# Kernel tuning notes

Measured on AMD Instinct MI355X. Metric: run time of the kernel, lower is better.

## Reference

```python
import jax, jax.numpy as jnp
import numpy as np

B, X, Y, Z, CIN = 4, 64, 64, 64, 32
COUT = 32
MX, MY, MZ = 16, 16, 16


def setup_inputs() -> dict:
    key = jax.random.key(0)
    k1, k2, k3 = jax.random.split(key, 3)
    x = jax.random.normal(k1, (B, X, Y, Z, CIN), dtype=jnp.float32)
    # Glorot-uniform-like scale for (in, out, mx, my, mz) weights
    fan = CIN + COUT
    lim = np.sqrt(6.0 / fan).astype(np.float32)
    w_real = jax.random.uniform(k2, (CIN, COUT, MX, MY, MZ), minval=-lim, maxval=lim, dtype=jnp.float32)
    w_imag = jax.random.uniform(k3, (CIN, COUT, MX, MY, MZ), minval=-lim, maxval=lim, dtype=jnp.float32)
    return {"x": x, "w_real": w_real, "w_imag": w_imag}


def reference(x, w_real, w_imag):
    # tf.signal.fft3d transforms the innermost 3 axes of the 5D input:
    # x is [B, X, Y, Z, C] so the FFT runs over (Y, Z, C) -- faithful to source.
    x_ft = jnp.fft.fftn(x.astype(jnp.complex64), axes=(-3, -2, -1))
    x_ft = jnp.transpose(x_ft, (0, 4, 1, 2, 3))            # [B, C, X, Y, Z]
    mx, my, mz = w_real.shape[2], w_real.shape[3], w_real.shape[4]
    x_crop = x_ft[:, :, :mx, :my, :mz]                     # [B, Cin, mx, my, mz]
    w = jax.lax.complex(w_real, w_imag)                    # [Cin, Cout, mx, my, mz]
    out_ft = jnp.einsum('bixyz,ioxyz->boxyz', x_crop, w)   # [B, Cout, mx, my, mz]
    sx, sy, sz = x.shape[1], x.shape[2], x.shape[3]
    out_ft = jnp.pad(out_ft, ((0, 0), (0, 0), (0, sx - mx), (0, sy - my), (0, sz - mz)))
    out_ft = jnp.transpose(out_ft, (0, 2, 3, 4, 1))        # [B, X, Y, Z, Cout]
    x_out = jnp.fft.ifftn(out_ft, axes=(-3, -2, -1))
    return jnp.real(x_out)
```

## Files before the change

### kernel.cpp

```cpp
#include <hip/hip_runtime.h>
#include <math.h>

#define PI_F 3.14159265358979323846f


__global__ __launch_bounds__(256) void k_dft_z(const float* __restrict__ x,
                                               float2* __restrict__ T1) {
    int bid = blockIdx.x;
    int ih = bid & 1, yg = (bid >> 1) & 7, xx = (bid >> 4) & 15, b = bid >> 8;
    __shared__ float  sx[8192];
    __shared__ float2 twt[1024];
    float4* sx4 = (float4*)sx;
    const float4* src4 = (const float4*)(x + (size_t)((b * 64 + xx) * 64 + yg * 8) * 2048) + ih * 4;
    #pragma unroll
    for (int t = threadIdx.x; t < 2048; t += 256) {
        int i4 = t & 3, z = (t >> 2) & 63, y = t >> 8;
        sx4[(y * 64 + z) * 4 + i4] = src4[(size_t)y * 512 + z * 8 + i4];
    }
    const float cn = -2.0f * PI_F / 64.0f;
    for (int t = threadIdx.x; t < 1024; t += 256) {
        int z = t >> 4, kz = t & 15;
        float s, c; sincosf(cn * (float)((z * kz) & 63), &s, &c);
        twt[t] = make_float2(c, s);
    }
    __syncthreads();
    int ig = threadIdx.x & 3, kz2 = (threadIdx.x >> 2) & 7, y8 = threadIdx.x >> 5;
    float ar0[4], ai0[4], ar1[4], ai1[4];
    #pragma unroll
    for (int j = 0; j < 4; j++) { ar0[j] = ai0[j] = ar1[j] = ai1[j] = 0.f; }
    const float4* twv = (const float4*)twt;
    #pragma unroll 8
    for (int z = 0; z < 64; z++) {
        float4 va = sx4[(y8 * 64 + z) * 4 + ig];
        float4 tp = twv[z * 8 + kz2];
        float v[4] = {va.x, va.y, va.z, va.w};
        #pragma unroll
        for (int j = 0; j < 4; j++) {
            ar0[j] = fmaf(v[j], tp.x, ar0[j]);
            ai0[j] = fmaf(v[j], tp.y, ai0[j]);
            ar1[j] = fmaf(v[j], tp.z, ar1[j]);
            ai1[j] = fmaf(v[j], tp.w, ai1[j]);
        }
    }
    int y = yg * 8 + y8, kz0 = kz2 * 2, i0 = ih * 16 + ig * 4;
    float2* dst = T1 + (size_t)((b * 16 + xx) * 64 + y) * 512;
    float4* d0 = (float4*)(dst + kz0 * 32 + i0);
    d0[0] = make_float4(ar0[0], ai0[0], ar0[1], ai0[1]);
    d0[1] = make_float4(ar0[2], ai0[2], ar0[3], ai0[3]);
    float4* d1 = (float4*)(dst + (kz0 + 1) * 32 + i0);
    d1[0] = make_float4(ar1[0], ai1[0], ar1[1], ai1[1]);
    d1[1] = make_float4(ar1[2], ai1[2], ar1[3], ai1[3]);
}

__global__ __launch_bounds__(256) void k_dft_y(const float2* __restrict__ T1,
                                               float2* __restrict__ XH) {
    int bid = blockIdx.x;
    int ih = bid & 1, kzg = (bid >> 1) & 3, xx = (bid >> 3) & 15, b = bid >> 7;
    __shared__ float4 sT4[2304];
    __shared__ float2 twt[1024];
    const float4* Tg4 = (const float4*)T1;
    size_t gbase = (size_t)(b * 16 + xx) * 64 * 256;
    #pragma unroll
    for (int t = threadIdx.x; t < 2048; t += 256) {
        int i4 = t & 7, kz4 = (t >> 3) & 3, y = t >> 5;
        sT4[kz4 * 576 + y * 9 + i4] =
            Tg4[gbase + (size_t)y * 256 + (kzg * 4 + kz4) * 16 + ih * 8 + i4];
    }
    const float cn = -2.0f * PI_F / 64.0f;
    for (int t = threadIdx.x; t < 1024; t += 256) {
        int y = t >> 4, ky = t & 15;
        float s, c; sincosf(cn * (float)((y * ky) & 63), &s, &c);
        twt[t] = make_float2(c, s);
    }
    __syncthreads();
    int ig = threadIdx.x & 7, ky2 = (threadIdx.x >> 3) & 7, kz4 = threadIdx.x >> 6;
    float ar[2][2], ai[2][2];
    #pragma unroll
    for (int h = 0; h < 2; h++) { ar[h][0] = ar[h][1] = ai[h][0] = ai[h][1] = 0.f; }
    const float4* twv = (const float4*)twt;
    #pragma unroll 8
    for (int y = 0; y < 64; y++) {
        float4 a  = sT4[kz4 * 576 + y * 9 + ig];
        float4 tp = twv[y * 8 + ky2];
        float xr[2] = {a.x, a.z}, xi[2] = {a.y, a.w};
        #pragma unroll
        for (int j = 0; j < 2; j++) {
            ar[0][j] += xr[j] * tp.x - xi[j] * tp.y;
            ai[0][j] += xr[j] * tp.y + xi[j] * tp.x;
            ar[1][j] += xr[j] * tp.z - xi[j] * tp.w;
            ai[1][j] += xr[j] * tp.w + xi[j] * tp.z;
        }
    }
    int kz = kzg * 4 + kz4;
    #pragma unroll
    for (int h = 0; h < 2; h++) {
        int ky = ky2 * 2 + h;
        float2* dp = XH + (((size_t)(b * 16 + xx) * 16 + ky) * 16 + kz) * 32 + ih * 16 + ig * 2;
        *(float4*)dp = make_float4(ar[h][0], ai[h][0], ar[h][1], ai[h][1]);
    }
}

__global__ __launch_bounds__(512) void k_mid(const float2* __restrict__ XH,
                                             const float* __restrict__ wr,
                                             const float* __restrict__ wi,
                                             float2* __restrict__ G,
                                             float* __restrict__ out) {
    int bid = blockIdx.x;
    if (bid >= 256) {
        int f = bid - 256;
        int b = f / 384, rem = f - b * 384;
        float4* d4 = (float4*)(out + (size_t)(b * 64 + 16) * 131072) + (size_t)rem * 4096;
        #pragma unroll
        for (int r = 0; r < 8; ++r)
            d4[r * 512 + threadIdx.x] = make_float4(0.f, 0.f, 0.f, 0.f);
        return;
    }
    int ky = bid & 15, xx = bid >> 4;
    __shared__ float2 sA[4 * 528];
    __shared__ float2 sB[4 * 576];
    __shared__ float2 twt[1024];
    for (int t = threadIdx.x; t < 2048; t += 512) {
        int b = t >> 9, kz = (t >> 5) & 15, i = t & 31;
        sA[b * 528 + kz * 33 + i] =
            XH[(((size_t)(b * 16 + xx) * 16 + ky) * 16 + kz) * 32 + i];
    }
    const float cn32 = -2.0f * PI_F / 32.0f;
    for (int t = threadIdx.x; t < 1024; t += 512) {
        int m = t >> 5, k = t & 31;
        float s, c; sincosf(cn32 * (float)((m * k) & 31), &s, &c);
        twt[t] = make_float2(c, s);
    }
    __syncthreads();
    const float4* twv = (const float4*)twt;
    {
        int kz = threadIdx.x & 15, kig = (threadIdx.x >> 4) & 7, b = threadIdx.x >> 7;
        float xr[4], xi[4];
        #pragma unroll
        for (int j = 0; j < 4; j++) { xr[j] = xi[j] = 0.f; }
        #pragma unroll 8
        for (int i = 0; i < 32; i++) {
            float2 a   = sA[b * 528 + kz * 33 + i];
            float4 tp0 = twv[i * 16 + kig * 2];
            float4 tp1 = twv[i * 16 + kig * 2 + 1];
            xr[0] += a.x * tp0.x - a.y * tp0.y;  xi[0] += a.x * tp0.y + a.y * tp0.x;
            xr[1] += a.x * tp0.z - a.y * tp0.w;  xi[1] += a.x * tp0.w + a.y * tp0.z;
            xr[2] += a.x * tp1.x - a.y * tp1.y;  xi[2] += a.x * tp1.y + a.y * tp1.x;
            xr[3] += a.x * tp1.z - a.y * tp1.w;  xi[3] += a.x * tp1.w + a.y * tp1.z;
        }
        #pragma unroll
        for (int j = 0; j < 4; j++)
            sB[b * 576 + (kig * 4 + j) * 18 + kz] = make_float2(xr[j], xi[j]);
    }
    __syncthreads();
    {
        int kzg = threadIdx.x & 3, o = (threadIdx.x >> 2) & 31, b = threadIdx.x >> 7;
        int wbase = xx * 256 + ky * 16 + kzg * 4;
        float Fr[4], Fi[4];
        #pragma unroll
        for (int q = 0; q < 4; q++) { Fr[q] = Fi[q] = 0.f; }
        const float4* sB4 = (const float4*)sB;
        #pragma unroll 4
        for (int ki = 0; ki < 32; ki++) {
            float4 a01 = sB4[b * 288 + ki * 9 + kzg * 2];
            float4 a23 = sB4[b * 288 + ki * 9 + kzg * 2 + 1];
            float4 w4r = *(const float4*)(wr + (size_t)(ki * 32 + o) * 4096 + wbase);
            float4 w4i = *(const float4*)(wi + (size_t)(ki * 32 + o) * 4096 + wbase);
            float xr[4]  = {a01.x, a01.z, a23.x, a23.z};
            float xi[4]  = {a01.y, a01.w, a23.y, a23.w};
            float wrv[4] = {w4r.x, w4r.y, w4r.z, w4r.w};
            float wiv[4] = {w4i.x, w4i.y, w4i.z, w4i.w};
            #pragma unroll
            for (int q = 0; q < 4; q++) {
                Fr[q] += xr[q] * wrv[q] - xi[q] * wiv[q];
                Fi[q] += xr[q] * wiv[q] + xi[q] * wrv[q];
            }
        }
        #pragma unroll
        for (int q = 0; q < 4; q++) {
            int kz = kzg * 4 + q;
            sA[b * 528 + kz * 33 + o] = make_float2(Fr[q], Fi[q]);
        }
    }
    __syncthreads();
    {
        int kz = threadIdx.x & 15, cog = (threadIdx.x >> 4) & 7, b = threadIdx.x >> 7;
        float gr[4], gi[4];
        #pragma unroll
        for (int j = 0; j < 4; j++) { gr[j] = gi[j] = 0.f; }
        #pragma unroll 8
        for (int o = 0; o < 32; o++) {
            float2 f   = sA[b * 528 + kz * 33 + o];
            float4 tp0 = twv[o * 16 + cog * 2];
            float4 tp1 = twv[o * 16 + cog * 2 + 1];
            gr[0] += f.x * tp0.x + f.y * tp0.y;  gi[0] += f.y * tp0.x - f.x * tp0.y;
            gr[1] += f.x * tp0.z + f.y * tp0.w;  gi[1] += f.y * tp0.z - f.x * tp0.w;
            gr[2] += f.x * tp1.x + f.y * tp1.y;  gi[2] += f.y * tp1.x - f.x * tp1.y;
            gr[3] += f.x * tp1.z + f.y * tp1.w;  gi[3] += f.y * tp1.z - f.x * tp1.w;
        }
        float2* dp = G + (((size_t)(b * 16 + xx) * 16 + ky) * 16 + kz) * 32 + cog * 4;
        ((float4*)dp)[0] = make_float4(gr[0], gi[0], gr[1], gi[1]);
        ((float4*)dp)[1] = make_float4(gr[2], gi[2], gr[3], gi[3]);
    }
}

__global__ __launch_bounds__(256) void k_idft_zy(const float2* __restrict__ G,
                                                 float* __restrict__ out) {
    int bid = blockIdx.x;
    int ch = bid & 1, zc = (bid >> 1) & 7, xx = (bid >> 4) & 15, b = bid >> 8;
    float* dstb = out + (size_t)(b * 64 + xx) * 131072;
    __shared__ float2 sH[128 * 18];
    __shared__ float2 twy[1024];
    __shared__ float2 twz[8 * 17];
    const float cp = 2.0f * PI_F / 64.0f;
    for (int t = threadIdx.x; t < 1024; t += 256) {
        int ky = t >> 6, y = t & 63;
        float s, c; sincosf(cp * (float)((ky * y) & 63), &s, &c);
        twy[t] = make_float2(c, s);
    }
    if (threadIdx.x < 128) {
        int dz = threadIdx.x >> 4, kz = threadIdx.x & 15;
        int z = zc * 8 + dz;
        float s, c; sincosf(cp * (float)((kz * z) & 63), &s, &c);
        twz[dz * 17 + kz] = make_float2(c, s);
    }
    __syncthreads();
    {
        int coq = threadIdx.x & 1, dz = (threadIdx.x >> 1) & 7, ky = threadIdx.x >> 4;
        const float2* Gb = G + ((size_t)(b * 16 + xx) * 16 + ky) * 512 + ch * 16 + coq * 8;
        float Hr[8], Hi[8];
        #pragma unroll
        for (int j = 0; j < 8; j++) { Hr[j] = Hi[j] = 0.f; }
        #pragma unroll 4
        for (int kz = 0; kz < 16; kz++) {
            float2 tz = twz[dz * 17 + kz];
            #pragma unroll
            for (int k = 0; k < 4; k++) {
                float4 g = *(const float4*)(Gb + kz * 32 + k * 2);
                Hr[2 * k]     += g.x * tz.x - g.y * tz.y;
                Hi[2 * k]     += g.x * tz.y + g.y * tz.x;
                Hr[2 * k + 1] += g.z * tz.x - g.w * tz.y;
                Hi[2 * k + 1] += g.z * tz.y + g.w * tz.x;
            }
        }
        float2* hp = sH + (ky * 8 + dz) * 18 + coq * 8;
        #pragma unroll
        for (int k = 0; k < 4; k++)
            *(float4*)(hp + k * 2) = make_float4(Hr[2 * k], Hi[2 * k], Hr[2 * k + 1], Hi[2 * k + 1]);
    }
    __syncthreads();
    {
        int cog = threadIdx.x & 1, dz = (threadIdx.x >> 1) & 7, yg = threadIdx.x >> 4;
        float acc[4][8];
        #pragma unroll
        for (int yl = 0; yl < 4; yl++)
            #pragma unroll
            for (int cl = 0; cl < 8; cl++) acc[yl][cl] = 0.f;
        const float4* twy4 = (const float4*)twy;
        const float4* sH4 = (const float4*)sH;
        for (int ky = 0; ky < 16; ky++) {
            float4 t0 = twy4[ky * 32 + yg * 2 + 0];
            float4 t1 = twy4[ky * 32 + yg * 2 + 1];
            float4 h0 = sH4[(ky * 8 + dz) * 9 + cog * 4 + 0];
            float4 h1 = sH4[(ky * 8 + dz) * 9 + cog * 4 + 1];
            float4 h2 = sH4[(ky * 8 + dz) * 9 + cog * 4 + 2];
            float4 h3 = sH4[(ky * 8 + dz) * 9 + cog * 4 + 3];
            float tc[4] = {t0.x, t0.z, t1.x, t1.z};
            float ts[4] = {t0.y, t0.w, t1.y, t1.w};
            float hr[8] = {h0.x, h0.z, h1.x, h1.z, h2.x, h2.z, h3.x, h3.z};
            float hi[8] = {h0.y, h0.w, h1.y, h1.w, h2.y, h2.w, h3.y, h3.w};
            #pragma unroll
            for (int yl = 0; yl < 4; yl++)
                #pragma unroll
                for (int cl = 0; cl < 8; cl++)
                    acc[yl][cl] += tc[yl] * hr[cl] - ts[yl] * hi[cl];
        }
        const float sc = 1.0f / 131072.0f;
        #pragma unroll
        for (int yl = 0; yl < 4; yl++) {
            int y = yg * 4 + yl;
            float4* d4 = (float4*)(dstb + ((size_t)y * 64 + zc * 8 + dz) * 32 + ch * 16 + cog * 8);
            d4[0] = make_float4(acc[yl][0] * sc, acc[yl][1] * sc, acc[yl][2] * sc, acc[yl][3] * sc);
            d4[1] = make_float4(acc[yl][4] * sc, acc[yl][5] * sc, acc[yl][6] * sc, acc[yl][7] * sc);
        }
    }
}

extern "C" void kernel_launch(void* const* d_in, const int* in_sizes, int n_in,
                              void* d_out, int out_size, void* d_ws, size_t ws_size,
                              hipStream_t stream) {
    const float* x  = (const float*)d_in[0];
    const float* wr = (const float*)d_in[1];
    const float* wi = (const float*)d_in[2];
    float* out = (float*)d_out;
    char*  ws  = (char*)d_ws;
    float2* T1 = (float2*)ws;
    float2* XH = (float2*)(ws + (size_t)16777216);
    float2* Gb = (float2*)(ws + (size_t)16777216 + 4194304);

    k_dft_z  <<<1024, 256, 0, stream>>>(x, T1);
    k_dft_y  <<< 512, 256, 0, stream>>>(T1, XH);
    k_mid    <<<1792, 512, 0, stream>>>(XH, wr, wi, Gb, out);
    k_idft_zy<<<1024, 256, 0, stream>>>(Gb, out);
}
```

Baseline: 288.8 us.

## Use fast trig intrinsics for twiddles and remap idft_zy z-stage threads

Replaces sincosf with __cosf/__sinf when building twiddle tables in every kernel, which makes table setup cheaper at some cost in accuracy. In k_idft_zy, the first stage is remapped so each thread handles one output channel across 8 ky values. The kz twiddles are cached in registers and global G reads become coalesced per channel. The sH shared buffer is shrunk to a stride of 17 float2 to avoid bank conflicts, so the second stage now reads float2 instead of float4.

```diff
diff --git a/kernel.cpp b/kernel.cpp
--- a/kernel.cpp
+++ b/kernel.cpp
@@ -20,8 +20,8 @@
     const float cn = -2.0f * PI_F / 64.0f;
     for (int t = threadIdx.x; t < 1024; t += 256) {
         int z = t >> 4, kz = t & 15;
-        float s, c; sincosf(cn * (float)((z * kz) & 63), &s, &c);
-        twt[t] = make_float2(c, s);
+        float a = cn * (float)((z * kz) & 63);
+        twt[t] = make_float2(__cosf(a), __sinf(a));
     }
     __syncthreads();
     int ig = threadIdx.x & 3, kz2 = (threadIdx.x >> 2) & 7, y8 = threadIdx.x >> 5;
@@ -69,8 +69,8 @@
     const float cn = -2.0f * PI_F / 64.0f;
     for (int t = threadIdx.x; t < 1024; t += 256) {
         int y = t >> 4, ky = t & 15;
-        float s, c; sincosf(cn * (float)((y * ky) & 63), &s, &c);
-        twt[t] = make_float2(c, s);
+        float a = cn * (float)((y * ky) & 63);
+        twt[t] = make_float2(__cosf(a), __sinf(a));
     }
     __syncthreads();
     int ig = threadIdx.x & 7, ky2 = (threadIdx.x >> 3) & 7, kz4 = threadIdx.x >> 6;
@@ -127,8 +127,8 @@
     const float cn32 = -2.0f * PI_F / 32.0f;
     for (int t = threadIdx.x; t < 1024; t += 512) {
         int m = t >> 5, k = t & 31;
-        float s, c; sincosf(cn32 * (float)((m * k) & 31), &s, &c);
-        twt[t] = make_float2(c, s);
+        float a = cn32 * (float)((m * k) & 31);
+        twt[t] = make_float2(__cosf(a), __sinf(a));
     }
     __syncthreads();
     const float4* twv = (const float4*)twt;
@@ -208,44 +208,44 @@
     int bid = blockIdx.x;
     int ch = bid & 1, zc = (bid >> 1) & 7, xx = (bid >> 4) & 15, b = bid >> 8;
     float* dstb = out + (size_t)(b * 64 + xx) * 131072;
-    __shared__ float2 sH[128 * 18];
+    __shared__ float2 sH[128 * 17];
     __shared__ float2 twy[1024];
     __shared__ float2 twz[8 * 17];
     const float cp = 2.0f * PI_F / 64.0f;
     for (int t = threadIdx.x; t < 1024; t += 256) {
         int ky = t >> 6, y = t & 63;
-        float s, c; sincosf(cp * (float)((ky * y) & 63), &s, &c);
-        twy[t] = make_float2(c, s);
+        float a = cp * (float)((ky * y) & 63);
+        twy[t] = make_float2(__cosf(a), __sinf(a));
     }
     if (threadIdx.x < 128) {
         int dz = threadIdx.x >> 4, kz = threadIdx.x & 15;
         int z = zc * 8 + dz;
-        float s, c; sincosf(cp * (float)((kz * z) & 63), &s, &c);
-        twz[dz * 17 + kz] = make_float2(c, s);
-    }
-    __syncthreads();
-    {
-        int coq = threadIdx.x & 1, dz = (threadIdx.x >> 1) & 7, ky = threadIdx.x >> 4;
-        const float2* Gb = G + ((size_t)(b * 16 + xx) * 16 + ky) * 512 + ch * 16 + coq * 8;
-        float Hr[8], Hi[8];
-        #pragma unroll
-        for (int j = 0; j < 8; j++) { Hr[j] = Hi[j] = 0.f; }
-        #pragma unroll 4
-        for (int kz = 0; kz < 16; kz++) {
-            float2 tz = twz[dz * 17 + kz];
-            #pragma unroll
-            for (int k = 0; k < 4; k++) {
-                float4 g = *(const float4*)(Gb + kz * 32 + k * 2);
-                Hr[2 * k]     += g.x * tz.x - g.y * tz.y;
-                Hi[2 * k]     += g.x * tz.y + g.y * tz.x;
-                Hr[2 * k + 1] += g.z * tz.x - g.w * tz.y;
-                Hi[2 * k + 1] += g.z * tz.y + g.w * tz.x;
+        float a = cp * (float)((kz * z) & 63);
+        twz[dz * 17 + kz] = make_float2(__cosf(a), __sinf(a));
+    }
+    __syncthreads();
+    {
+        int co = threadIdx.x & 15, dz = (threadIdx.x >> 4) & 7, kyg = threadIdx.x >> 7;
+        float tzc[16], tzs[16];
+        #pragma unroll
+        for (int kz = 0; kz < 16; ++kz) {
+            float2 t = twz[dz * 17 + kz];
+            tzc[kz] = t.x; tzs[kz] = t.y;
+        }
+        const float2* Gb0 = G + (size_t)(b * 16 + xx) * 16 * 512 + ch * 16 + co;
+        #pragma unroll
+        for (int t = 0; t < 8; ++t) {
+            int ky = kyg * 8 + t;
+            const float2* Gk = Gb0 + (size_t)ky * 512;
+            float hr = 0.f, hi = 0.f;
+            #pragma unroll
+            for (int kz = 0; kz < 16; ++kz) {
+                float2 g = Gk[kz * 32];
+                hr += g.x * tzc[kz] - g.y * tzs[kz];
+                hi += g.x * tzs[kz] + g.y * tzc[kz];
             }
-        }
-        float2* hp = sH + (ky * 8 + dz) * 18 + coq * 8;
-        #pragma unroll
-        for (int k = 0; k < 4; k++)
-            *(float4*)(hp + k * 2) = make_float4(Hr[2 * k], Hi[2 * k], Hr[2 * k + 1], Hi[2 * k + 1]);
+            sH[(ky * 8 + dz) * 17 + co] = make_float2(hr, hi);
+        }
     }
     __syncthreads();
     {
@@ -256,18 +256,18 @@
             #pragma unroll
             for (int cl = 0; cl < 8; cl++) acc[yl][cl] = 0.f;
         const float4* twy4 = (const float4*)twy;
-        const float4* sH4 = (const float4*)sH;
         for (int ky = 0; ky < 16; ky++) {
             float4 t0 = twy4[ky * 32 + yg * 2 + 0];
             float4 t1 = twy4[ky * 32 + yg * 2 + 1];
-            float4 h0 = sH4[(ky * 8 + dz) * 9 + cog * 4 + 0];
-            float4 h1 = sH4[(ky * 8 + dz) * 9 + cog * 4 + 1];
-            float4 h2 = sH4[(ky * 8 + dz) * 9 + cog * 4 + 2];
-            float4 h3 = sH4[(ky * 8 + dz) * 9 + cog * 4 + 3];
+            const float2* hp = sH + (ky * 8 + dz) * 17 + cog * 8;
+            float hr[8], hi[8];
+            #pragma unroll
+            for (int cl = 0; cl < 8; ++cl) {
+                float2 h = hp[cl];
+                hr[cl] = h.x; hi[cl] = h.y;
+            }
             float tc[4] = {t0.x, t0.z, t1.x, t1.z};
             float ts[4] = {t0.y, t0.w, t1.y, t1.w};
-            float hr[8] = {h0.x, h0.z, h1.x, h1.z, h2.x, h2.z, h3.x, h3.z};
-            float hi[8] = {h0.y, h0.w, h1.y, h1.w, h2.y, h2.w, h3.y, h3.w};
             #pragma unroll
             for (int yl = 0; yl < 4; yl++)
                 #pragma unroll
```

Result: slower. 312.7 us (+8.3%).
